# Optimization experiments

Measured on AMD Instinct MI355X. Metric: run time of the kernel, lower is better.

## Reference

```python
import jax, jax.numpy as jnp
import numpy as np

ALPHA = 100.0
EPS = 1e-12  # matches torch F.normalize eps


def l2norm(v, axis):
    n = jnp.linalg.norm(v, axis=axis, keepdims=True)
    return v / jnp.maximum(n, EPS)


def setup_inputs() -> dict:
    key = jax.random.key(0)
    k1, k2 = jax.random.split(key)
    x = jax.random.normal(k1, (32, 512, 32, 32), dtype=jnp.float32)
    vocabs = jax.random.uniform(k2, (64, 512), dtype=jnp.float32)  # torch.rand init
    return {"x": x, "vocabs": vocabs}


def reference(x, vocabs):
    # x: [N, C, H, W]; vocabs: [K, C]
    N, C, H, W = x.shape
    K = vocabs.shape[0]
    x = l2norm(x, axis=1)                       # normalize descriptors over C
    xf = x.reshape(N, C, H * W)                 # [N, C, P]

    # 1x1 conv with weight = 2*alpha*vocabs, bias = -alpha*||vocabs||
    w = 2.0 * ALPHA * vocabs                    # [K, C]
    b = -ALPHA * jnp.linalg.norm(vocabs, axis=1)  # [K]
    logits = jnp.einsum('ncp,kc->nkp', xf, w) + b[None, :, None]
    a = jax.nn.softmax(logits, axis=1)          # soft assignment over K

    # Distributive rewrite of sum_p a[n,k,p]*(x[n,c,p] - vocabs[k,c])
    vlad = jnp.einsum('nkp,ncp->nkc', a, xf) - a.sum(-1)[:, :, None] * vocabs[None]
    vlad = l2norm(vlad, axis=2)                 # intra-normalization
    vlad = vlad.reshape(N, K * C)
    return l2norm(vlad, axis=1)
```

## Files before the change

kernel.cpp:

```cpp
#include <hip/hip_runtime.h>
#include <math.h>
#include <stdint.h>

#define ALPHA 100.0f
#define EPSN 1e-12f

typedef __attribute__((ext_vector_type(8))) short bf16x8;
typedef __attribute__((ext_vector_type(16))) float f32x16;
typedef __attribute__((ext_vector_type(4))) unsigned int u32x4;

static __device__ __forceinline__ unsigned int f2bf(float f) {
    unsigned int u = __builtin_bit_cast(unsigned int, f);
    return (u + 0x7FFFu + ((u >> 16) & 1u)) >> 16;
}
static __device__ __forceinline__ float bf2f(unsigned int b) {
    return __builtin_bit_cast(float, b << 16);
}

__global__ __launch_bounds__(64) void prep_kernel(const float* __restrict__ v,
                                                  unsigned short* __restrict__ vh,
                                                  unsigned short* __restrict__ vl,
                                                  float* __restrict__ bias) {
    int k = blockIdx.x, lane = threadIdx.x;
    const float* row = v + k * 512;
    float ssq = 0.f;
#pragma unroll
    for (int i = 0; i < 8; ++i) {
        int c = lane + 64 * i;
        float f = row[c];
        ssq = fmaf(f, f, ssq);
        unsigned int hi = f2bf(f);
        unsigned int lo = f2bf(f - bf2f(hi));
        vh[k * 512 + c] = (unsigned short)hi;
        vl[k * 512 + c] = (unsigned short)lo;
    }
#pragma unroll
    for (int off = 32; off > 0; off >>= 1) ssq += __shfl_xor(ssq, off, 64);
    if (lane == 0) bias[k] = -ALPHA * sqrtf(ssq);
}

__global__ __launch_bounds__(256) void assign_kernel(
    const float* __restrict__ x, const unsigned short* __restrict__ vh,
    const unsigned short* __restrict__ vl, const float* __restrict__ bias,
    unsigned short* __restrict__ aT, float* __restrict__ asum,
    float* __restrict__ sinv_g) {
    __shared__ __align__(16) uint32_t xt[32 * 130];
    __shared__ __align__(16) uint32_t vt_h[64 * 20];
    __shared__ __align__(16) uint32_t vt_l[64 * 20];
    __shared__ float ssq_lds[256];
    __shared__ float bias_l[64];

    int tid = threadIdx.x, bx = blockIdx.x;
    int n = bx >> 3;
    int pblk = (bx & 7) << 7;
    int lane = tid & 63, w = tid >> 6, h = lane >> 5, cl = lane & 31;

    if (tid < 64) bias_l[tid] = bias[tid];

    const float* xg = x + (size_t)n * 524288 + pblk;
    int ps = tid & 127;
    int chalf = tid >> 7;
    int ks = tid >> 2, js = tid & 3;

    f32x16 acc0, acc1;
#pragma unroll
    for (int r = 0; r < 16; ++r) { acc0[r] = 0.f; acc1[r] = 0.f; }
    float ssq = 0.f;

    float px[16];
    u32x4 pvh, pvl;
#pragma unroll
    for (int i = 0; i < 16; ++i)
        px[i] = xg[(size_t)(chalf + 2 * i) * 1024 + ps];
    pvh = *(const u32x4*)(vh + ks * 512 + js * 8);
    pvl = *(const u32x4*)(vl + ks * 512 + js * 8);

    for (int ch = 0; ch < 16; ++ch) {
        __syncthreads();
#pragma unroll
        for (int i = 0; i < 16; ++i) {
            float f = px[i];
            ssq = fmaf(f, f, ssq);
            unsigned int hi = f2bf(f);
            unsigned int lo = f2bf(f - bf2f(hi));
            xt[(chalf + 2 * i) * 130 + ps] = (hi << 16) | lo;
        }
        *(u32x4*)&vt_h[ks * 20 + js * 4] = pvh;
        *(u32x4*)&vt_l[ks * 20 + js * 4] = pvl;
        __syncthreads();
        if (ch < 15) {
            int c0 = (ch + 1) * 32;
#pragma unroll
            for (int i = 0; i < 16; ++i)
                px[i] = xg[(size_t)(c0 + chalf + 2 * i) * 1024 + ps];
            pvh = *(const u32x4*)(vh + ks * 512 + c0 + js * 8);
            pvl = *(const u32x4*)(vl + ks * 512 + c0 + js * 8);
        }
#pragma unroll
        for (int s = 0; s < 2; ++s) {
            bf16x8 ah0 = *(const bf16x8*)&vt_h[cl * 20 + 8 * s + 4 * h];
            bf16x8 ah1 = *(const bf16x8*)&vt_h[(cl + 32) * 20 + 8 * s + 4 * h];
            bf16x8 al0 = *(const bf16x8*)&vt_l[cl * 20 + 8 * s + 4 * h];
            bf16x8 al1 = *(const bf16x8*)&vt_l[(cl + 32) * 20 + 8 * s + 4 * h];
            uint32_t wv[8];
#pragma unroll
            for (int j = 0; j < 8; ++j)
                wv[j] = xt[(16 * s + 8 * h + j) * 130 + w * 32 + cl];
            u32x4 bhp, blp;
#pragma unroll
            for (int i = 0; i < 4; ++i) {
                bhp[i] = (wv[2 * i] >> 16) | (wv[2 * i + 1] & 0xFFFF0000u);
                blp[i] = (wv[2 * i] & 0xFFFFu) | (wv[2 * i + 1] << 16);
            }
            bf16x8 bh = __builtin_bit_cast(bf16x8, bhp);
            bf16x8 bl = __builtin_bit_cast(bf16x8, blp);
            acc0 = __builtin_amdgcn_mfma_f32_32x32x16_bf16(ah0, bh, acc0, 0, 0, 0);
            acc1 = __builtin_amdgcn_mfma_f32_32x32x16_bf16(ah1, bh, acc1, 0, 0, 0);
            acc0 = __builtin_amdgcn_mfma_f32_32x32x16_bf16(ah0, bl, acc0, 0, 0, 0);
            acc1 = __builtin_amdgcn_mfma_f32_32x32x16_bf16(ah1, bl, acc1, 0, 0, 0);
            acc0 = __builtin_amdgcn_mfma_f32_32x32x16_bf16(al0, bh, acc0, 0, 0, 0);
            acc1 = __builtin_amdgcn_mfma_f32_32x32x16_bf16(al1, bh, acc1, 0, 0, 0);
        }
    }
    ssq_lds[tid] = ssq;
    __syncthreads();

    int p_l = w * 32 + cl;
    float ssqv = ssq_lds[p_l] + ssq_lds[p_l + 128];
    float sv = 1.0f / fmaxf(sqrtf(ssqv), EPSN);
    if (h == 0) sinv_g[n * 1024 + pblk + p_l] = sv;
    float twoAs = 2.0f * ALPHA * sv;
    float e[2][16];
    float m = -INFINITY;
#pragma unroll
    for (int t = 0; t < 2; ++t)
#pragma unroll
        for (int r = 0; r < 16; ++r) {
            int k = (r & 3) + 8 * (r >> 2) + 4 * h + 32 * t;
            float lv = fmaf(twoAs, (t ? acc1[r] : acc0[r]), bias_l[k]);
            e[t][r] = lv;
            m = fmaxf(m, lv);
        }
    m = fmaxf(m, __shfl_xor(m, 32, 64));
    float s = 0.f;
#pragma unroll
    for (int t = 0; t < 2; ++t)
#pragma unroll
        for (int r = 0; r < 16; ++r) {
            e[t][r] = expf(e[t][r] - m);
            s += e[t][r];
        }
    s += __shfl_xor(s, 32, 64);
    float rs = 1.0f / s;
    unsigned short* aTn = aT + (size_t)n * 65536 + pblk + p_l;
#pragma unroll
    for (int t = 0; t < 2; ++t)
#pragma unroll
        for (int r = 0; r < 16; ++r) {
            int k = (r & 3) + 8 * (r >> 2) + 4 * h + 32 * t;
            float a = e[t][r] * rs;
            aTn[(size_t)k * 1024] = (unsigned short)f2bf(a);
            float red = a;
#pragma unroll
            for (int off = 1; off <= 16; off <<= 1) red += __shfl_xor(red, off, 64);
            if (cl == 0) atomicAdd(&asum[n * 64 + k], red);
        }
}

__global__ __launch_bounds__(256) void vlad_kernel(
    const float* __restrict__ x, const unsigned short* __restrict__ aT,
    const float* __restrict__ sinv_g, const float* __restrict__ asum,
    const float* __restrict__ vocabs, float* __restrict__ out,
    float* __restrict__ knorm) {
    __shared__ __align__(16) uint32_t xt[64 * 36];
    __shared__ __align__(16) uint32_t at[64 * 36];
    __shared__ float sinv_l[1024];
    __shared__ float asum_l[64];

    int tid = threadIdx.x, bx = blockIdx.x;
    int n = bx >> 3;
    int cblk = (bx & 7) << 6;
    int lane = tid & 63, w = tid >> 6, h = lane >> 5, cl = lane & 31;
    int wk = w & 1, wc = w >> 1;

    ((float4*)sinv_l)[tid] = ((const float4*)(sinv_g + n * 1024))[tid];
    if (tid < 64) asum_l[tid] = asum[n * 64 + tid];

    int ph = tid & 31;
    int cs = tid >> 5;
    int ks = tid >> 2, js = tid & 3;

    const float* xg = x + (size_t)n * 524288 + (size_t)cblk * 1024;
    const unsigned short* ag = aT + (size_t)n * 65536;

    f32x16 acc;
#pragma unroll
    for (int r = 0; r < 16; ++r) acc[r] = 0.f;

    float2 qx[8];
    u32x4 qa0, qa1;
#pragma unroll
    for (int i = 0; i < 8; ++i)
        qx[i] = *(const float2*)(xg + (size_t)(cs + 8 * i) * 1024 + 2 * ph);
    qa0 = *(const u32x4*)(ag + ks * 1024 + js * 16);
    qa1 = *(const u32x4*)(ag + ks * 1024 + js * 16 + 8);
    __syncthreads();

    for (int chp = 0; chp < 16; ++chp) {
        int p0 = chp * 64;
        float s0 = sinv_l[p0 + 2 * ph];
        float s1 = sinv_l[p0 + 2 * ph + 1];
#pragma unroll
        for (int i = 0; i < 8; ++i) {
            unsigned int b0 = f2bf(qx[i].x * s0);
            unsigned int b1 = f2bf(qx[i].y * s1);
            xt[(cs + 8 * i) * 36 + ph] = b0 | (b1 << 16);
        }
        *(u32x4*)&at[ks * 36 + js * 8] = qa0;
        *(u32x4*)&at[ks * 36 + js * 8 + 4] = qa1;
        __syncthreads();
        if (chp < 15) {
            int p1 = p0 + 64;
#pragma unroll
            for (int i = 0; i < 8; ++i)
                qx[i] = *(const float2*)(xg + (size_t)(cs + 8 * i) * 1024 + p1 + 2 * ph);
            qa0 = *(const u32x4*)(ag + ks * 1024 + p1 + js * 16);
            qa1 = *(const u32x4*)(ag + ks * 1024 + p1 + js * 16 + 8);
        }
#pragma unroll
        for (int s = 0; s < 4; ++s) {
            bf16x8 af = *(const bf16x8*)&at[(32 * wk + cl) * 36 + 8 * s + 4 * h];
            bf16x8 bf = *(const bf16x8*)&xt[(32 * wc + cl) * 36 + 8 * s + 4 * h];
            acc = __builtin_amdgcn_mfma_f32_32x32x16_bf16(af, bf, acc, 0, 0, 0);
        }
        __syncthreads();
    }
#pragma unroll
    for (int r = 0; r < 16; ++r) {
        int k = (r & 3) + 8 * (r >> 2) + 4 * h + 32 * wk;
        int c = cblk + 32 * wc + cl;
        float val = fmaf(-asum_l[k], vocabs[k * 512 + c], acc[r]);
        out[(size_t)n * 32768 + (size_t)k * 512 + c] = val;
        float t2 = val * val;
#pragma unroll
        for (int off = 1; off <= 16; off <<= 1) t2 += __shfl_xor(t2, off, 64);
        if (cl == 0) atomicAdd(&knorm[n * 64 + k], t2);
    }
}

__global__ __launch_bounds__(256) void scale_kernel(float* __restrict__ out,
                                                    const float* __restrict__ knorm) {
    int n = blockIdx.y;
    int sb = blockIdx.x;
    int tid = threadIdx.x;
    __shared__ float sc[64];
    __shared__ float tots;
    if (tid < 64) {
        float kn = knorm[n * 64 + tid];
        float nk = sqrtf(kn);
        float inv = 1.0f / fmaxf(nk, EPSN);
        sc[tid] = inv;
        float t = nk * inv;
        float t2 = t * t;
#pragma unroll
        for (int off = 32; off > 0; off >>= 1) t2 += __shfl_xor(t2, off, 64);
        if (tid == 0) tots = t2;
    }
    __syncthreads();
    float invt = 1.0f / fmaxf(sqrtf(tots), EPSN);
    float* base = out + (size_t)n * 32768 + sb * 4096;
#pragma unroll
    for (int i = 0; i < 16; ++i) {
        int idx = tid + 256 * i;
        int k = (sb * 4096 + idx) >> 9;
        base[idx] *= sc[k] * invt;
    }
}

extern "C" void kernel_launch(void* const* d_in, const int* in_sizes, int n_in,
                              void* d_out, int out_size, void* d_ws, size_t ws_size,
                              hipStream_t stream) {
    const float* x = (const float*)d_in[0];
    const float* vocabs = (const float*)d_in[1];
    float* out = (float*)d_out;
    char* ws = (char*)d_ws;
    unsigned short* vh = (unsigned short*)(ws);
    unsigned short* vl = (unsigned short*)(ws + 65536);
    float* bias  = (float*)(ws + 131072);
    float* asum  = (float*)(ws + 131328);
    float* knorm = (float*)(ws + 139520);
    float* sinv  = (float*)(ws + 147712);
    unsigned short* aT = (unsigned short*)(ws + 278784);

    hipMemsetAsync(asum, 0, 16384, stream);
    prep_kernel<<<64, 64, 0, stream>>>(vocabs, vh, vl, bias);
    assign_kernel<<<256, 256, 0, stream>>>(x, vh, vl, bias, aT, asum, sinv);
    vlad_kernel<<<256, 256, 0, stream>>>(x, aT, sinv, asum, vocabs, out, knorm);
    scale_kernel<<<dim3(8, 32), 256, 0, stream>>>(out, knorm);
}
```

Measured before the change: 143.5 us.

## Give each wave a private LDS tile and drop block barriers in assign and vlad

```diff
diff --git a/kernel.cpp b/kernel.cpp
--- a/kernel.cpp
+++ b/kernel.cpp
@@ -9,12 +9,23 @@
 typedef __attribute__((ext_vector_type(16))) float f32x16;
 typedef __attribute__((ext_vector_type(4))) unsigned int u32x4;
 
-static __device__ __forceinline__ unsigned int f2bf(float f) {
-    unsigned int u = __builtin_bit_cast(unsigned int, f);
+static __device__ __forceinline__ uint32_t f2bf(float f) {
+    uint32_t u = __builtin_bit_cast(uint32_t, f);
     return (u + 0x7FFFu + ((u >> 16) & 1u)) >> 16;
 }
-static __device__ __forceinline__ float bf2f(unsigned int b) {
-    return __builtin_bit_cast(float, b << 16);
+static __device__ __forceinline__ float bfhi(uint32_t u) {
+    return __builtin_bit_cast(float, u & 0xFFFF0000u);
+}
+static __device__ __forceinline__ float bflo(uint32_t u) {
+    return __builtin_bit_cast(float, u << 16);
+}
+static __device__ __forceinline__ uint32_t stage1(float f) {
+    uint32_t hi = f2bf(f);
+    uint32_t lo = f2bf(f - __builtin_bit_cast(float, hi << 16));
+    return (hi << 16) | lo;
+}
+static __device__ __forceinline__ uint32_t packbf(float a, float b) {
+    return f2bf(a) | (f2bf(b) << 16);
 }
 
 __global__ __launch_bounds__(64) void prep_kernel(const float* __restrict__ v,
@@ -29,14 +40,72 @@
         int c = lane + 64 * i;
         float f = row[c];
         ssq = fmaf(f, f, ssq);
-        unsigned int hi = f2bf(f);
-        unsigned int lo = f2bf(f - bf2f(hi));
+        uint32_t hi = f2bf(f);
+        uint32_t lo = f2bf(f - __builtin_bit_cast(float, hi << 16));
         vh[k * 512 + c] = (unsigned short)hi;
         vl[k * 512 + c] = (unsigned short)lo;
     }
 #pragma unroll
     for (int off = 32; off > 0; off >>= 1) ssq += __shfl_xor(ssq, off, 64);
     if (lane == 0) bias[k] = -ALPHA * sqrtf(ssq);
+}
+
+static __device__ __forceinline__ void assign_body(
+    int i, float4 (&pxc)[4], u32x4 (&qvc)[8], u32x4 (&qvn)[8],
+    f32x16& acc0, f32x16& acc1, float& ssq, uint32_t* xwp,
+    const float* xg, const unsigned short* vhr0, const unsigned short* vhr1,
+    const unsigned short* vlr0, const unsigned short* vlr1,
+    int crow, int p4, int h, int cl) {
+#pragma unroll
+    for (int k = 0; k < 4; ++k) {
+        float4 v = pxc[k];
+        int idx = (8 * k + crow) * 34 + p4;
+        *(uint2*)&xwp[idx] = make_uint2(stage1(v.x), stage1(v.y));
+        *(uint2*)&xwp[idx + 2] = make_uint2(stage1(v.z), stage1(v.w));
+    }
+    int cpre = ((i + 2) & 15) * 32;
+#pragma unroll
+    for (int k = 0; k < 4; ++k)
+        pxc[k] = *(const float4*)(xg + (size_t)(cpre + 8 * k + crow) * 1024 + p4);
+    int co = ((i + 1) & 15) * 32 + 8 * h;
+    qvn[0] = *(const u32x4*)(vhr0 + co);
+    qvn[1] = *(const u32x4*)(vhr1 + co);
+    qvn[2] = *(const u32x4*)(vlr0 + co);
+    qvn[3] = *(const u32x4*)(vlr1 + co);
+    qvn[4] = *(const u32x4*)(vhr0 + co + 16);
+    qvn[5] = *(const u32x4*)(vhr1 + co + 16);
+    qvn[6] = *(const u32x4*)(vlr0 + co + 16);
+    qvn[7] = *(const u32x4*)(vlr1 + co + 16);
+#pragma unroll
+    for (int s = 0; s < 2; ++s) {
+        bf16x8 ah0 = __builtin_bit_cast(bf16x8, qvc[4 * s + 0]);
+        bf16x8 ah1 = __builtin_bit_cast(bf16x8, qvc[4 * s + 1]);
+        bf16x8 al0 = __builtin_bit_cast(bf16x8, qvc[4 * s + 2]);
+        bf16x8 al1 = __builtin_bit_cast(bf16x8, qvc[4 * s + 3]);
+        uint32_t wv[8];
+#pragma unroll
+        for (int j = 0; j < 8; ++j)
+            wv[j] = xwp[(16 * s + 8 * h + j) * 34 + cl];
+#pragma unroll
+        for (int j = 0; j < 8; ++j) {
+            float xr = bfhi(wv[j]) + bflo(wv[j]);
+            ssq = fmaf(xr, xr, ssq);
+        }
+        u32x4 bhp, blp;
+#pragma unroll
+        for (int q = 0; q < 4; ++q) {
+            bhp[q] = (wv[2 * q] >> 16) | (wv[2 * q + 1] & 0xFFFF0000u);
+            blp[q] = (wv[2 * q] & 0xFFFFu) | (wv[2 * q + 1] << 16);
+        }
+        bf16x8 bh = __builtin_bit_cast(bf16x8, bhp);
+        bf16x8 bl = __builtin_bit_cast(bf16x8, blp);
+        acc0 = __builtin_amdgcn_mfma_f32_32x32x16_bf16(ah0, bh, acc0, 0, 0, 0);
+        acc1 = __builtin_amdgcn_mfma_f32_32x32x16_bf16(ah1, bh, acc1, 0, 0, 0);
+        acc0 = __builtin_amdgcn_mfma_f32_32x32x16_bf16(ah0, bl, acc0, 0, 0, 0);
+        acc1 = __builtin_amdgcn_mfma_f32_32x32x16_bf16(ah1, bl, acc1, 0, 0, 0);
+        acc0 = __builtin_amdgcn_mfma_f32_32x32x16_bf16(al0, bh, acc0, 0, 0, 0);
+        acc1 = __builtin_amdgcn_mfma_f32_32x32x16_bf16(al1, bh, acc1, 0, 0, 0);
+    }
 }
 
 __global__ __launch_bounds__(256) void assign_kernel(
@@ -44,90 +113,54 @@
     const unsigned short* __restrict__ vl, const float* __restrict__ bias,
     unsigned short* __restrict__ aT, float* __restrict__ asum,
     float* __restrict__ sinv_g) {
-    __shared__ __align__(16) uint32_t xt[32 * 130];
-    __shared__ __align__(16) uint32_t vt_h[64 * 20];
-    __shared__ __align__(16) uint32_t vt_l[64 * 20];
-    __shared__ float ssq_lds[256];
+    __shared__ uint32_t xw[4][32 * 34];
     __shared__ float bias_l[64];
-
     int tid = threadIdx.x, bx = blockIdx.x;
-    int n = bx >> 3;
-    int pblk = (bx & 7) << 7;
-    int lane = tid & 63, w = tid >> 6, h = lane >> 5, cl = lane & 31;
-
+    int n = bx >> 3, pblk = (bx & 7) << 7;
+    int l = tid & 63, w = tid >> 6, h = l >> 5, cl = l & 31;
     if (tid < 64) bias_l[tid] = bias[tid];
-
-    const float* xg = x + (size_t)n * 524288 + pblk;
-    int ps = tid & 127;
-    int chalf = tid >> 7;
-    int ks = tid >> 2, js = tid & 3;
+    const float* xg = x + (size_t)n * 524288 + pblk + 32 * w;
+    int crow = l >> 3, p4 = (l & 7) << 2;
+    const unsigned short* vhr0 = vh + cl * 512;
+    const unsigned short* vhr1 = vh + (cl + 32) * 512;
+    const unsigned short* vlr0 = vl + cl * 512;
+    const unsigned short* vlr1 = vl + (cl + 32) * 512;
+    uint32_t* xwp = xw[w];
 
     f32x16 acc0, acc1;
 #pragma unroll
     for (int r = 0; r < 16; ++r) { acc0[r] = 0.f; acc1[r] = 0.f; }
     float ssq = 0.f;
 
-    float px[16];
-    u32x4 pvh, pvl;
-#pragma unroll
-    for (int i = 0; i < 16; ++i)
-        px[i] = xg[(size_t)(chalf + 2 * i) * 1024 + ps];
-    pvh = *(const u32x4*)(vh + ks * 512 + js * 8);
-    pvl = *(const u32x4*)(vl + ks * 512 + js * 8);
-
-    for (int ch = 0; ch < 16; ++ch) {
-        __syncthreads();
-#pragma unroll
-        for (int i = 0; i < 16; ++i) {
-            float f = px[i];
-            ssq = fmaf(f, f, ssq);
-            unsigned int hi = f2bf(f);
-            unsigned int lo = f2bf(f - bf2f(hi));
-            xt[(chalf + 2 * i) * 130 + ps] = (hi << 16) | lo;
-        }
-        *(u32x4*)&vt_h[ks * 20 + js * 4] = pvh;
-        *(u32x4*)&vt_l[ks * 20 + js * 4] = pvl;
-        __syncthreads();
-        if (ch < 15) {
-            int c0 = (ch + 1) * 32;
-#pragma unroll
-            for (int i = 0; i < 16; ++i)
-                px[i] = xg[(size_t)(c0 + chalf + 2 * i) * 1024 + ps];
-            pvh = *(const u32x4*)(vh + ks * 512 + c0 + js * 8);
-            pvl = *(const u32x4*)(vl + ks * 512 + c0 + js * 8);
-        }
-#pragma unroll
-        for (int s = 0; s < 2; ++s) {
-            bf16x8 ah0 = *(const bf16x8*)&vt_h[cl * 20 + 8 * s + 4 * h];
-            bf16x8 ah1 = *(const bf16x8*)&vt_h[(cl + 32) * 20 + 8 * s + 4 * h];
-            bf16x8 al0 = *(const bf16x8*)&vt_l[cl * 20 + 8 * s + 4 * h];
-            bf16x8 al1 = *(const bf16x8*)&vt_l[(cl + 32) * 20 + 8 * s + 4 * h];
-            uint32_t wv[8];
-#pragma unroll
-            for (int j = 0; j < 8; ++j)
-                wv[j] = xt[(16 * s + 8 * h + j) * 130 + w * 32 + cl];
-            u32x4 bhp, blp;
-#pragma unroll
-            for (int i = 0; i < 4; ++i) {
-                bhp[i] = (wv[2 * i] >> 16) | (wv[2 * i + 1] & 0xFFFF0000u);
-                blp[i] = (wv[2 * i] & 0xFFFFu) | (wv[2 * i + 1] << 16);
-            }
-            bf16x8 bh = __builtin_bit_cast(bf16x8, bhp);
-            bf16x8 bl = __builtin_bit_cast(bf16x8, blp);
-            acc0 = __builtin_amdgcn_mfma_f32_32x32x16_bf16(ah0, bh, acc0, 0, 0, 0);
-            acc1 = __builtin_amdgcn_mfma_f32_32x32x16_bf16(ah1, bh, acc1, 0, 0, 0);
-            acc0 = __builtin_amdgcn_mfma_f32_32x32x16_bf16(ah0, bl, acc0, 0, 0, 0);
-            acc1 = __builtin_amdgcn_mfma_f32_32x32x16_bf16(ah1, bl, acc1, 0, 0, 0);
-            acc0 = __builtin_amdgcn_mfma_f32_32x32x16_bf16(al0, bh, acc0, 0, 0, 0);
-            acc1 = __builtin_amdgcn_mfma_f32_32x32x16_bf16(al1, bh, acc1, 0, 0, 0);
-        }
-    }
-    ssq_lds[tid] = ssq;
+    float4 px0[4], px1[4];
+    u32x4 qv0[8], qv1[8];
+#pragma unroll
+    for (int k = 0; k < 4; ++k) {
+        px0[k] = *(const float4*)(xg + (size_t)(8 * k + crow) * 1024 + p4);
+        px1[k] = *(const float4*)(xg + (size_t)(32 + 8 * k + crow) * 1024 + p4);
+    }
+    {
+        int co = 8 * h;
+        qv0[0] = *(const u32x4*)(vhr0 + co);
+        qv0[1] = *(const u32x4*)(vhr1 + co);
+        qv0[2] = *(const u32x4*)(vlr0 + co);
+        qv0[3] = *(const u32x4*)(vlr1 + co);
+        qv0[4] = *(const u32x4*)(vhr0 + co + 16);
+        qv0[5] = *(const u32x4*)(vhr1 + co + 16);
+        qv0[6] = *(const u32x4*)(vlr0 + co + 16);
+        qv0[7] = *(const u32x4*)(vlr1 + co + 16);
+    }
+    for (int ii = 0; ii < 16; ii += 2) {
+        assign_body(ii, px0, qv0, qv1, acc0, acc1, ssq, xwp, xg,
+                    vhr0, vhr1, vlr0, vlr1, crow, p4, h, cl);
+        assign_body(ii + 1, px1, qv1, qv0, acc0, acc1, ssq, xwp, xg,
+                    vhr0, vhr1, vlr0, vlr1, crow, p4, h, cl);
+    }
     __syncthreads();
 
-    int p_l = w * 32 + cl;
-    float ssqv = ssq_lds[p_l] + ssq_lds[p_l + 128];
+    float ssqv = ssq + __shfl_xor(ssq, 32, 64);
     float sv = 1.0f / fmaxf(sqrtf(ssqv), EPSN);
+    int p_l = 32 * w + cl;
     if (h == 0) sinv_g[n * 1024 + pblk + p_l] = sv;
     float twoAs = 2.0f * ALPHA * sv;
     float e[2][16];
@@ -167,73 +200,78 @@
         }
 }
 
+static __device__ __forceinline__ void vlad_body(
+    int i, float4 (&qxc)[8], u32x4 (&qac)[4], u32x4 (&qan)[4], f32x16& acc,
+    uint32_t* xwp, const float* xg, const unsigned short* ag,
+    const float* sinv_l, int crow, int p16, int h, int cl) {
+    int p0 = i << 6;
+    float4 sv4 = *(const float4*)&sinv_l[p0 + p16];
+#pragma unroll
+    for (int k = 0; k < 8; ++k) {
+        float4 v = qxc[k];
+        int idx = (4 * k + crow) * 34 + (p16 >> 1);
+        *(uint2*)&xwp[idx] = make_uint2(packbf(v.x * sv4.x, v.y * sv4.y),
+                                        packbf(v.z * sv4.z, v.w * sv4.w));
+    }
+    int ppre = ((i + 2) & 15) << 6;
+#pragma unroll
+    for (int k = 0; k < 8; ++k)
+        qxc[k] = *(const float4*)(xg + (size_t)(4 * k + crow) * 1024 + ppre + p16);
+    int pnext = ((i + 1) & 15) << 6;
+#pragma unroll
+    for (int s = 0; s < 4; ++s)
+        qan[s] = *(const u32x4*)(ag + pnext + 16 * s);
+#pragma unroll
+    for (int s = 0; s < 4; ++s) {
+        bf16x8 af = __builtin_bit_cast(bf16x8, qac[s]);
+        uint2 r0 = *(const uint2*)&xwp[cl * 34 + 8 * s + 4 * h];
+        uint2 r1 = *(const uint2*)&xwp[cl * 34 + 8 * s + 4 * h + 2];
+        u32x4 bb;
+        bb[0] = r0.x; bb[1] = r0.y; bb[2] = r1.x; bb[3] = r1.y;
+        acc = __builtin_amdgcn_mfma_f32_32x32x16_bf16(
+            af, __builtin_bit_cast(bf16x8, bb), acc, 0, 0, 0);
+    }
+}
+
 __global__ __launch_bounds__(256) void vlad_kernel(
     const float* __restrict__ x, const unsigned short* __restrict__ aT,
     const float* __restrict__ sinv_g, const float* __restrict__ asum,
     const float* __restrict__ vocabs, float* __restrict__ out,
     float* __restrict__ knorm) {
-    __shared__ __align__(16) uint32_t xt[64 * 36];
-    __shared__ __align__(16) uint32_t at[64 * 36];
+    __shared__ uint32_t xw[4][32 * 34];
     __shared__ float sinv_l[1024];
     __shared__ float asum_l[64];
-
     int tid = threadIdx.x, bx = blockIdx.x;
-    int n = bx >> 3;
-    int cblk = (bx & 7) << 6;
-    int lane = tid & 63, w = tid >> 6, h = lane >> 5, cl = lane & 31;
+    int n = (bx & 7) * 4 + (bx >> 6);
+    int cblk = ((bx >> 3) & 7) << 6;
+    int l = tid & 63, w = tid >> 6, h = l >> 5, cl = l & 31;
     int wk = w & 1, wc = w >> 1;
-
     ((float4*)sinv_l)[tid] = ((const float4*)(sinv_g + n * 1024))[tid];
     if (tid < 64) asum_l[tid] = asum[n * 64 + tid];
-
-    int ph = tid & 31;
-    int cs = tid >> 5;
-    int ks = tid >> 2, js = tid & 3;
-
-    const float* xg = x + (size_t)n * 524288 + (size_t)cblk * 1024;
-    const unsigned short* ag = aT + (size_t)n * 65536;
+    __syncthreads();
+
+    const float* xg = x + (size_t)n * 524288 + (size_t)(cblk + 32 * wc) * 1024;
+    const unsigned short* ag = aT + (size_t)n * 65536 + (32 * wk + cl) * 1024 + 8 * h;
+    int crow = l >> 4, p16 = (l & 15) << 2;
+    uint32_t* xwp = xw[w];
 
     f32x16 acc;
 #pragma unroll
     for (int r = 0; r < 16; ++r) acc[r] = 0.f;
 
-    float2 qx[8];
-    u32x4 qa0, qa1;
-#pragma unroll
-    for (int i = 0; i < 8; ++i)
-        qx[i] = *(const float2*)(xg + (size_t)(cs + 8 * i) * 1024 + 2 * ph);
-    qa0 = *(const u32x4*)(ag + ks * 1024 + js * 16);
-    qa1 = *(const u32x4*)(ag + ks * 1024 + js * 16 + 8);
-    __syncthreads();
-
-    for (int chp = 0; chp < 16; ++chp) {
-        int p0 = chp * 64;
-        float s0 = sinv_l[p0 + 2 * ph];
-        float s1 = sinv_l[p0 + 2 * ph + 1];
-#pragma unroll
-        for (int i = 0; i < 8; ++i) {
-            unsigned int b0 = f2bf(qx[i].x * s0);
-            unsigned int b1 = f2bf(qx[i].y * s1);
-            xt[(cs + 8 * i) * 36 + ph] = b0 | (b1 << 16);
-        }
-        *(u32x4*)&at[ks * 36 + js * 8] = qa0;
-        *(u32x4*)&at[ks * 36 + js * 8 + 4] = qa1;
-        __syncthreads();
-        if (chp < 15) {
-            int p1 = p0 + 64;
-#pragma unroll
-            for (int i = 0; i < 8; ++i)
-                qx[i] = *(const float2*)(xg + (size_t)(cs + 8 * i) * 1024 + p1 + 2 * ph);
-            qa0 = *(const u32x4*)(ag + ks * 1024 + p1 + js * 16);
-            qa1 = *(const u32x4*)(ag + ks * 1024 + p1 + js * 16 + 8);
-        }
-#pragma unroll
-        for (int s = 0; s < 4; ++s) {
-            bf16x8 af = *(const bf16x8*)&at[(32 * wk + cl) * 36 + 8 * s + 4 * h];
-            bf16x8 bf = *(const bf16x8*)&xt[(32 * wc + cl) * 36 + 8 * s + 4 * h];
-            acc = __builtin_amdgcn_mfma_f32_32x32x16_bf16(af, bf, acc, 0, 0, 0);
-        }
-        __syncthreads();
+    float4 qx0[8], qx1[8];
+    u32x4 qa0[4], qa1[4];
+#pragma unroll
+    for (int k = 0; k < 8; ++k) {
+        qx0[k] = *(const float4*)(xg + (size_t)(4 * k + crow) * 1024 + p16);
+        qx1[k] = *(const float4*)(xg + (size_t)(4 * k + crow) * 1024 + 64 + p16);
+    }
+#pragma unroll
+    for (int s = 0; s < 4; ++s) qa0[s] = *(const u32x4*)(ag + 16 * s);
+
+    for (int ii = 0; ii < 16; ii += 2) {
+        vlad_body(ii, qx0, qa0, qa1, acc, xwp, xg, ag, sinv_l, crow, p16, h, cl);
+        vlad_body(ii + 1, qx1, qa1, qa0, acc, xwp, xg, ag, sinv_l, crow, p16, h, cl);
     }
 #pragma unroll
     for (int r = 0; r < 16; ++r) {
```

Measured after the change: 149.3 us. 1.04x slower.

## Double grid size, fold x-normalization into assignments, drop memset and sinv buffer

Applied to the files above, without the earlier changes.

```diff
diff --git a/kernel.cpp b/kernel.cpp
--- a/kernel.cpp
+++ b/kernel.cpp
@@ -9,19 +9,32 @@
 typedef __attribute__((ext_vector_type(16))) float f32x16;
 typedef __attribute__((ext_vector_type(4))) unsigned int u32x4;
 
-static __device__ __forceinline__ unsigned int f2bf(float f) {
-    unsigned int u = __builtin_bit_cast(unsigned int, f);
+static __device__ __forceinline__ uint32_t f2bf(float f) {
+    uint32_t u = __builtin_bit_cast(uint32_t, f);
     return (u + 0x7FFFu + ((u >> 16) & 1u)) >> 16;
 }
-static __device__ __forceinline__ float bf2f(unsigned int b) {
-    return __builtin_bit_cast(float, b << 16);
+static __device__ __forceinline__ float bfhi(uint32_t u) {
+    return __builtin_bit_cast(float, u & 0xFFFF0000u);
+}
+static __device__ __forceinline__ float bflo(uint32_t u) {
+    return __builtin_bit_cast(float, u << 16);
+}
+static __device__ __forceinline__ uint32_t stage1(float f) {
+    uint32_t hi = f2bf(f);
+    uint32_t lo = f2bf(f - __builtin_bit_cast(float, hi << 16));
+    return (hi << 16) | lo;
+}
+static __device__ __forceinline__ uint32_t packbf(float a, float b) {
+    return f2bf(a) | (f2bf(b) << 16);
 }
 
 __global__ __launch_bounds__(64) void prep_kernel(const float* __restrict__ v,
                                                   unsigned short* __restrict__ vh,
                                                   unsigned short* __restrict__ vl,
-                                                  float* __restrict__ bias) {
+                                                  float* __restrict__ bias,
+                                                  float* __restrict__ az) {
     int k = blockIdx.x, lane = threadIdx.x;
+    az[k * 64 + lane] = 0.f;
     const float* row = v + k * 512;
     float ssq = 0.f;
 #pragma unroll
@@ -29,8 +42,8 @@
         int c = lane + 64 * i;
         float f = row[c];
         ssq = fmaf(f, f, ssq);
-        unsigned int hi = f2bf(f);
-        unsigned int lo = f2bf(f - bf2f(hi));
+        uint32_t hi = f2bf(f);
+        uint32_t lo = f2bf(f - __builtin_bit_cast(float, hi << 16));
         vh[k * 512 + c] = (unsigned short)hi;
         vl[k * 512 + c] = (unsigned short)lo;
     }
@@ -42,209 +55,224 @@
 __global__ __launch_bounds__(256) void assign_kernel(
     const float* __restrict__ x, const unsigned short* __restrict__ vh,
     const unsigned short* __restrict__ vl, const float* __restrict__ bias,
-    unsigned short* __restrict__ aT, float* __restrict__ asum,
-    float* __restrict__ sinv_g) {
-    __shared__ __align__(16) uint32_t xt[32 * 130];
-    __shared__ __align__(16) uint32_t vt_h[64 * 20];
-    __shared__ __align__(16) uint32_t vt_l[64 * 20];
-    __shared__ float ssq_lds[256];
+    unsigned short* __restrict__ aT, float* __restrict__ asum) {
+    __shared__ uint32_t xs[32 * 66];
+    __shared__ uint32_t vhs[64 * 18];
+    __shared__ uint32_t vls[64 * 18];
     __shared__ float bias_l[64];
+    __shared__ float xch[2][2][32];
 
     int tid = threadIdx.x, bx = blockIdx.x;
-    int n = bx >> 3;
-    int pblk = (bx & 7) << 7;
-    int lane = tid & 63, w = tid >> 6, h = lane >> 5, cl = lane & 31;
+    int n = bx >> 4, pblk = (bx & 15) << 6;
+    int l = tid & 63, w = tid >> 6;
+    int kh = w & 1, ph = w >> 1;
+    int h = l >> 5, cl = l & 31;
 
     if (tid < 64) bias_l[tid] = bias[tid];
 
+    int xr = tid >> 4;
+    int xq = (tid & 15) << 2;
+    int vk = tid >> 2;
+    int vj = (tid & 3) << 3;
+
     const float* xg = x + (size_t)n * 524288 + pblk;
-    int ps = tid & 127;
-    int chalf = tid >> 7;
-    int ks = tid >> 2, js = tid & 3;
-
-    f32x16 acc0, acc1;
-#pragma unroll
-    for (int r = 0; r < 16; ++r) { acc0[r] = 0.f; acc1[r] = 0.f; }
+    const unsigned short* vhg = vh + vk * 512 + vj;
+    const unsigned short* vlg = vl + vk * 512 + vj;
+
+    f32x16 acc;
+#pragma unroll
+    for (int r = 0; r < 16; ++r) acc[r] = 0.f;
     float ssq = 0.f;
 
-    float px[16];
-    u32x4 pvh, pvl;
-#pragma unroll
-    for (int i = 0; i < 16; ++i)
-        px[i] = xg[(size_t)(chalf + 2 * i) * 1024 + ps];
-    pvh = *(const u32x4*)(vh + ks * 512 + js * 8);
-    pvl = *(const u32x4*)(vl + ks * 512 + js * 8);
+    float4 pxa = *(const float4*)(xg + (size_t)xr * 1024 + xq);
+    float4 pxb = *(const float4*)(xg + (size_t)(xr + 16) * 1024 + xq);
+    u32x4 pvh = *(const u32x4*)vhg;
+    u32x4 pvl = *(const u32x4*)vlg;
 
     for (int ch = 0; ch < 16; ++ch) {
         __syncthreads();
-#pragma unroll
-        for (int i = 0; i < 16; ++i) {
-            float f = px[i];
-            ssq = fmaf(f, f, ssq);
-            unsigned int hi = f2bf(f);
-            unsigned int lo = f2bf(f - bf2f(hi));
-            xt[(chalf + 2 * i) * 130 + ps] = (hi << 16) | lo;
-        }
-        *(u32x4*)&vt_h[ks * 20 + js * 4] = pvh;
-        *(u32x4*)&vt_l[ks * 20 + js * 4] = pvl;
+        *(uint2*)&xs[xr * 66 + xq] = make_uint2(stage1(pxa.x), stage1(pxa.y));
+        *(uint2*)&xs[xr * 66 + xq + 2] = make_uint2(stage1(pxa.z), stage1(pxa.w));
+        *(uint2*)&xs[(xr + 16) * 66 + xq] = make_uint2(stage1(pxb.x), stage1(pxb.y));
+        *(uint2*)&xs[(xr + 16) * 66 + xq + 2] = make_uint2(stage1(pxb.z), stage1(pxb.w));
+        int vb = vk * 18 + (vj >> 1);
+        *(uint2*)&vhs[vb] = make_uint2(pvh[0], pvh[1]);
+        *(uint2*)&vhs[vb + 2] = make_uint2(pvh[2], pvh[3]);
+        *(uint2*)&vls[vb] = make_uint2(pvl[0], pvl[1]);
+        *(uint2*)&vls[vb + 2] = make_uint2(pvl[2], pvl[3]);
         __syncthreads();
         if (ch < 15) {
-            int c0 = (ch + 1) * 32;
-#pragma unroll
-            for (int i = 0; i < 16; ++i)
-                px[i] = xg[(size_t)(c0 + chalf + 2 * i) * 1024 + ps];
-            pvh = *(const u32x4*)(vh + ks * 512 + c0 + js * 8);
-            pvl = *(const u32x4*)(vl + ks * 512 + c0 + js * 8);
+            int c0 = (ch + 1) << 5;
+            pxa = *(const float4*)(xg + (size_t)(c0 + xr) * 1024 + xq);
+            pxb = *(const float4*)(xg + (size_t)(c0 + xr + 16) * 1024 + xq);
+            pvh = *(const u32x4*)(vhg + c0);
+            pvl = *(const u32x4*)(vlg + c0);
         }
 #pragma unroll
         for (int s = 0; s < 2; ++s) {
-            bf16x8 ah0 = *(const bf16x8*)&vt_h[cl * 20 + 8 * s + 4 * h];
-            bf16x8 ah1 = *(const bf16x8*)&vt_h[(cl + 32) * 20 + 8 * s + 4 * h];
-            bf16x8 al0 = *(const bf16x8*)&vt_l[cl * 20 + 8 * s + 4 * h];
-            bf16x8 al1 = *(const bf16x8*)&vt_l[(cl + 32) * 20 + 8 * s + 4 * h];
+            int va = (32 * kh + cl) * 18 + 8 * s + 4 * h;
+            uint2 a0 = *(const uint2*)&vhs[va];
+            uint2 a1 = *(const uint2*)&vhs[va + 2];
+            uint2 b0 = *(const uint2*)&vls[va];
+            uint2 b1 = *(const uint2*)&vls[va + 2];
+            u32x4 ahp, alp;
+            ahp[0] = a0.x; ahp[1] = a0.y; ahp[2] = a1.x; ahp[3] = a1.y;
+            alp[0] = b0.x; alp[1] = b0.y; alp[2] = b1.x; alp[3] = b1.y;
             uint32_t wv[8];
 #pragma unroll
             for (int j = 0; j < 8; ++j)
-                wv[j] = xt[(16 * s + 8 * h + j) * 130 + w * 32 + cl];
+                wv[j] = xs[(16 * s + 8 * h + j) * 66 + 32 * ph + cl];
+#pragma unroll
+            for (int j = 0; j < 8; ++j) {
+                float xv = bfhi(wv[j]) + bflo(wv[j]);
+                ssq = fmaf(xv, xv, ssq);
+            }
             u32x4 bhp, blp;
 #pragma unroll
-            for (int i = 0; i < 4; ++i) {
-                bhp[i] = (wv[2 * i] >> 16) | (wv[2 * i + 1] & 0xFFFF0000u);
-                blp[i] = (wv[2 * i] & 0xFFFFu) | (wv[2 * i + 1] << 16);
+            for (int q = 0; q < 4; ++q) {
+                bhp[q] = (wv[2 * q] >> 16) | (wv[2 * q + 1] & 0xFFFF0000u);
+                blp[q] = (wv[2 * q] & 0xFFFFu) | (wv[2 * q + 1] << 16);
             }
+            bf16x8 ah = __builtin_bit_cast(bf16x8, ahp);
+            bf16x8 al = __builtin_bit_cast(bf16x8, alp);
             bf16x8 bh = __builtin_bit_cast(bf16x8, bhp);
             bf16x8 bl = __builtin_bit_cast(bf16x8, blp);
-            acc0 = __builtin_amdgcn_mfma_f32_32x32x16_bf16(ah0, bh, acc0, 0, 0, 0);
-            acc1 = __builtin_amdgcn_mfma_f32_32x32x16_bf16(ah1, bh, acc1, 0, 0, 0);
-            acc0 = __builtin_amdgcn_mfma_f32_32x32x16_bf16(ah0, bl, acc0, 0, 0, 0);
-            acc1 = __builtin_amdgcn_mfma_f32_32x32x16_bf16(ah1, bl, acc1, 0, 0, 0);
-            acc0 = __builtin_amdgcn_mfma_f32_32x32x16_bf16(al0, bh, acc0, 0, 0, 0);
-            acc1 = __builtin_amdgcn_mfma_f32_32x32x16_bf16(al1, bh, acc1, 0, 0, 0);
-        }
-    }
-    ssq_lds[tid] = ssq;
-    __syncthreads();
-
-    int p_l = w * 32 + cl;
-    float ssqv = ssq_lds[p_l] + ssq_lds[p_l + 128];
-    float sv = 1.0f / fmaxf(sqrtf(ssqv), EPSN);
-    if (h == 0) sinv_g[n * 1024 + pblk + p_l] = sv;
-    float twoAs = 2.0f * ALPHA * sv;
-    float e[2][16];
+            acc = __builtin_amdgcn_mfma_f32_32x32x16_bf16(ah, bh, acc, 0, 0, 0);
+            acc = __builtin_amdgcn_mfma_f32_32x32x16_bf16(ah, bl, acc, 0, 0, 0);
+            acc = __builtin_amdgcn_mfma_f32_32x32x16_bf16(al, bh, acc, 0, 0, 0);
+        }
+    }
+    ssq += __shfl_xor(ssq, 32, 64);
+    float sinv = 1.0f / fmaxf(sqrtf(ssq), EPSN);
+    float twoAs = 2.0f * ALPHA * sinv;
+    float e[16];
     float m = -INFINITY;
 #pragma unroll
-    for (int t = 0; t < 2; ++t)
-#pragma unroll
-        for (int r = 0; r < 16; ++r) {
-            int k = (r & 3) + 8 * (r >> 2) + 4 * h + 32 * t;
-            float lv = fmaf(twoAs, (t ? acc1[r] : acc0[r]), bias_l[k]);
-            e[t][r] = lv;
-            m = fmaxf(m, lv);
-        }
+    for (int r = 0; r < 16; ++r) {
+        int k = (r & 3) + 8 * (r >> 2) + 4 * h + 32 * kh;
+        float lv = fmaf(twoAs, acc[r], bias_l[k]);
+        e[r] = lv;
+        m = fmaxf(m, lv);
+    }
     m = fmaxf(m, __shfl_xor(m, 32, 64));
-    float s = 0.f;
-#pragma unroll
-    for (int t = 0; t < 2; ++t)
-#pragma unroll
-        for (int r = 0; r < 16; ++r) {
-            e[t][r] = expf(e[t][r] - m);
-            s += e[t][r];
-        }
-    s += __shfl_xor(s, 32, 64);
-    float rs = 1.0f / s;
-    unsigned short* aTn = aT + (size_t)n * 65536 + pblk + p_l;
-#pragma unroll
-    for (int t = 0; t < 2; ++t)
-#pragma unroll
-        for (int r = 0; r < 16; ++r) {
-            int k = (r & 3) + 8 * (r >> 2) + 4 * h + 32 * t;
-            float a = e[t][r] * rs;
-            aTn[(size_t)k * 1024] = (unsigned short)f2bf(a);
-            float red = a;
-#pragma unroll
-            for (int off = 1; off <= 16; off <<= 1) red += __shfl_xor(red, off, 64);
-            if (cl == 0) atomicAdd(&asum[n * 64 + k], red);
-        }
+    __syncthreads();
+    if (l < 32) xch[kh][ph][l] = m;
+    __syncthreads();
+    m = fmaxf(m, xch[1 - kh][ph][cl]);
+    float ssum = 0.f;
+#pragma unroll
+    for (int r = 0; r < 16; ++r) {
+        e[r] = expf(e[r] - m);
+        ssum += e[r];
+    }
+    ssum += __shfl_xor(ssum, 32, 64);
+    __syncthreads();
+    if (l < 32) xch[kh][ph][l] = ssum;
+    __syncthreads();
+    ssum += xch[1 - kh][ph][cl];
+    float rs = 1.0f / ssum;
+    float a2s = rs * sinv;
+    unsigned short* aTn = aT + (size_t)n * 65536 + pblk + 32 * ph + cl;
+#pragma unroll
+    for (int r = 0; r < 16; ++r) {
+        int k = (r & 3) + 8 * (r >> 2) + 4 * h + 32 * kh;
+        aTn[(size_t)k * 1024] = (unsigned short)f2bf(e[r] * a2s);
+        float red = e[r] * rs;
+#pragma unroll
+        for (int off = 1; off <= 16; off <<= 1) red += __shfl_xor(red, off, 64);
+        if (cl == 0) atomicAdd(&asum[n * 64 + k], red);
+    }
 }
 
 __global__ __launch_bounds__(256) void vlad_kernel(
     const float* __restrict__ x, const unsigned short* __restrict__ aT,
-    const float* __restrict__ sinv_g, const float* __restrict__ asum,
-    const float* __restrict__ vocabs, float* __restrict__ out,
-    float* __restrict__ knorm) {
-    __shared__ __align__(16) uint32_t xt[64 * 36];
-    __shared__ __align__(16) uint32_t at[64 * 36];
-    __shared__ float sinv_l[1024];
+    const float* __restrict__ asum, const float* __restrict__ vocabs,
+    float* __restrict__ out, float* __restrict__ knorm) {
+    __shared__ uint32_t xt[32 * 34];
+    __shared__ uint32_t at[64 * 34];
+    __shared__ float cmb[2][64][16];
     __shared__ float asum_l[64];
 
     int tid = threadIdx.x, bx = blockIdx.x;
-    int n = bx >> 3;
-    int cblk = (bx & 7) << 6;
-    int lane = tid & 63, w = tid >> 6, h = lane >> 5, cl = lane & 31;
-    int wk = w & 1, wc = w >> 1;
-
-    ((float4*)sinv_l)[tid] = ((const float4*)(sinv_g + n * 1024))[tid];
+    int n = bx >> 4, cb = (bx & 15) << 5;
+    int l = tid & 63, w = tid >> 6;
+    int kh = w & 1, ps = w >> 1;
+    int h = l >> 5, cl = l & 31;
+
     if (tid < 64) asum_l[tid] = asum[n * 64 + tid];
 
-    int ph = tid & 31;
-    int cs = tid >> 5;
-    int ks = tid >> 2, js = tid & 3;
-
-    const float* xg = x + (size_t)n * 524288 + (size_t)cblk * 1024;
-    const unsigned short* ag = aT + (size_t)n * 65536;
+    int xr = tid >> 3;
+    int xq = (tid & 7) << 2;
+    int ak = tid >> 2;
+    int aj = (tid & 3) << 4;
+
+    const float* xg = x + (size_t)n * 524288 + (size_t)(cb + xr) * 1024 + xq;
+    const unsigned short* ag = aT + (size_t)n * 65536 + (size_t)ak * 1024 + aj;
 
     f32x16 acc;
 #pragma unroll
     for (int r = 0; r < 16; ++r) acc[r] = 0.f;
 
-    float2 qx[8];
-    u32x4 qa0, qa1;
-#pragma unroll
-    for (int i = 0; i < 8; ++i)
-        qx[i] = *(const float2*)(xg + (size_t)(cs + 8 * i) * 1024 + 2 * ph);
-    qa0 = *(const u32x4*)(ag + ks * 1024 + js * 16);
-    qa1 = *(const u32x4*)(ag + ks * 1024 + js * 16 + 8);
-    __syncthreads();
-
-    for (int chp = 0; chp < 16; ++chp) {
-        int p0 = chp * 64;
-        float s0 = sinv_l[p0 + 2 * ph];
-        float s1 = sinv_l[p0 + 2 * ph + 1];
-#pragma unroll
-        for (int i = 0; i < 8; ++i) {
-            unsigned int b0 = f2bf(qx[i].x * s0);
-            unsigned int b1 = f2bf(qx[i].y * s1);
-            xt[(cs + 8 * i) * 36 + ph] = b0 | (b1 << 16);
-        }
-        *(u32x4*)&at[ks * 36 + js * 8] = qa0;
-        *(u32x4*)&at[ks * 36 + js * 8 + 4] = qa1;
+    float4 pxa = *(const float4*)xg;
+    float4 pxb = *(const float4*)(xg + 32);
+    u32x4 pa0 = *(const u32x4*)ag;
+    u32x4 pa1 = *(const u32x4*)(ag + 8);
+
+    for (int ch = 0; ch < 16; ++ch) {
         __syncthreads();
-        if (chp < 15) {
-            int p1 = p0 + 64;
-#pragma unroll
-            for (int i = 0; i < 8; ++i)
-                qx[i] = *(const float2*)(xg + (size_t)(cs + 8 * i) * 1024 + p1 + 2 * ph);
-            qa0 = *(const u32x4*)(ag + ks * 1024 + p1 + js * 16);
-            qa1 = *(const u32x4*)(ag + ks * 1024 + p1 + js * 16 + 8);
-        }
-#pragma unroll
-        for (int s = 0; s < 4; ++s) {
-            bf16x8 af = *(const bf16x8*)&at[(32 * wk + cl) * 36 + 8 * s + 4 * h];
-            bf16x8 bf = *(const bf16x8*)&xt[(32 * wc + cl) * 36 + 8 * s + 4 * h];
-            acc = __builtin_amdgcn_mfma_f32_32x32x16_bf16(af, bf, acc, 0, 0, 0);
-        }
+        int xb = xr * 34 + (xq >> 1);
+        *(uint2*)&xt[xb] = make_uint2(packbf(pxa.x, pxa.y), packbf(pxa.z, pxa.w));
+        *(uint2*)&xt[xb + 16] = make_uint2(packbf(pxb.x, pxb.y), packbf(pxb.z, pxb.w));
+        int ab = ak * 34 + (aj >> 1);
+        *(uint2*)&at[ab] = make_uint2(pa0[0], pa0[1]);
+        *(uint2*)&at[ab + 2] = make_uint2(pa0[2], pa0[3]);
+        *(uint2*)&at[ab + 4] = make_uint2(pa1[0], pa1[1]);
+        *(uint2*)&at[ab + 6] = make_uint2(pa1[2], pa1[3]);
         __syncthreads();
-    }
-#pragma unroll
-    for (int r = 0; r < 16; ++r) {
-        int k = (r & 3) + 8 * (r >> 2) + 4 * h + 32 * wk;
-        int c = cblk + 32 * wc + cl;
-        float val = fmaf(-asum_l[k], vocabs[k * 512 + c], acc[r]);
-        out[(size_t)n * 32768 + (size_t)k * 512 + c] = val;
-        float t2 = val * val;
-#pragma unroll
-        for (int off = 1; off <= 16; off <<= 1) t2 += __shfl_xor(t2, off, 64);
-        if (cl == 0) atomicAdd(&knorm[n * 64 + k], t2);
+        if (ch < 15) {
+            int p0 = (ch + 1) << 6;
+            pxa = *(const float4*)(xg + p0);
+            pxb = *(const float4*)(xg + p0 + 32);
+            pa0 = *(const u32x4*)(ag + p0);
+            pa1 = *(const u32x4*)(ag + p0 + 8);
+        }
+        if (ps == (ch & 1)) {
+#pragma unroll
+            for (int s = 0; s < 4; ++s) {
+                int va = (32 * kh + cl) * 34 + 8 * s + 4 * h;
+                uint2 f0 = *(const uint2*)&at[va];
+                uint2 f1 = *(const uint2*)&at[va + 2];
+                int vb = cl * 34 + 8 * s + 4 * h;
+                uint2 g0 = *(const uint2*)&xt[vb];
+                uint2 g1 = *(const uint2*)&xt[vb + 2];
+                u32x4 afp, bfp;
+                afp[0] = f0.x; afp[1] = f0.y; afp[2] = f1.x; afp[3] = f1.y;
+                bfp[0] = g0.x; bfp[1] = g0.y; bfp[2] = g1.x; bfp[3] = g1.y;
+                acc = __builtin_amdgcn_mfma_f32_32x32x16_bf16(
+                    __builtin_bit_cast(bf16x8, afp),
+                    __builtin_bit_cast(bf16x8, bfp), acc, 0, 0, 0);
+            }
+        }
+    }
+    __syncthreads();
+    if (ps == 1) {
+#pragma unroll
+        for (int r = 0; r < 16; ++r) cmb[kh][l][r] = acc[r];
+    }
+    __syncthreads();
+    if (ps == 0) {
+#pragma unroll
+        for (int r = 0; r < 16; ++r) {
+            int k = (r & 3) + 8 * (r >> 2) + 4 * h + 32 * kh;
+            int c = cb + cl;
+            float val = acc[r] + cmb[kh][l][r];
+            val = fmaf(-asum_l[k], vocabs[k * 512 + c], val);
+            out[(size_t)n * 32768 + (size_t)k * 512 + c] = val;
+            float t2 = val * val;
+#pragma unroll
+            for (int off = 1; off <= 16; off <<= 1) t2 += __shfl_xor(t2, off, 64);
+            if (cl == 0) atomicAdd(&knorm[n * 64 + k], t2);
+        }
     }
 }
 
@@ -289,12 +317,10 @@
     float* bias  = (float*)(ws + 131072);
     float* asum  = (float*)(ws + 131328);
     float* knorm = (float*)(ws + 139520);
-    float* sinv  = (float*)(ws + 147712);
-    unsigned short* aT = (unsigned short*)(ws + 278784);
-
-    hipMemsetAsync(asum, 0, 16384, stream);
-    prep_kernel<<<64, 64, 0, stream>>>(vocabs, vh, vl, bias);
-    assign_kernel<<<256, 256, 0, stream>>>(x, vh, vl, bias, aT, asum, sinv);
-    vlad_kernel<<<256, 256, 0, stream>>>(x, aT, sinv, asum, vocabs, out, knorm);
+    unsigned short* aT = (unsigned short*)(ws + 147712);
+
+    prep_kernel<<<64, 64, 0, stream>>>(vocabs, vh, vl, bias, asum);
+    assign_kernel<<<512, 256, 0, stream>>>(x, vh, vl, bias, aT, asum);
+    vlad_kernel<<<512, 256, 0, stream>>>(x, aT, asum, vocabs, out, knorm);
     scale_kernel<<<dim3(8, 32), 256, 0, stream>>>(out, knorm);
 }
```

After: 139.7 us. 1.03x faster.
